# Kernel optimization log

Measured on AMD Instinct MI355X. Metric: run time of the kernel, lower is better.

Reference implementation:

```python
import jax, jax.numpy as jnp
import numpy as np

B, N, K, NB = 8, 4096, 16, 8
MAX_RADIUS = 10.0
OUT_MUL = 64  # irreps_out = '64x1o' -> output dim 64*3 = 192


def setup_inputs() -> dict:
    key = jax.random.key(0)
    k1, k2 = jax.random.split(key)
    coords = jax.random.normal(k1, (B, N, 3), dtype=jnp.float32)
    tp_weight = jax.random.normal(k2, (1, NB, OUT_MUL), dtype=jnp.float32)
    return {"coords": coords, "tp_weight": tp_weight}


def _knn_indices(coords, k):
    # coords: [B, N, 3] -> nbr idx [B, N, k] (no self loops), per-batch kNN
    n = coords.shape[1]
    d2 = jnp.sum((coords[:, :, None, :] - coords[:, None, :, :]) ** 2, axis=-1)  # [B,N,N]
    d2 = jnp.where(jnp.eye(n, dtype=bool)[None], jnp.inf, d2)
    _, idx = jax.lax.top_k(-d2, k)  # k nearest
    return idx


def reference(coords, tp_weight):
    nbr = _knn_indices(coords, K)                                # [B,N,K] int32
    nbr_coords = jax.vmap(lambda c, i: c[i])(coords, nbr)        # [B,N,K,3]
    r = nbr_coords - coords[:, :, None, :]                       # sender - receiver
    dist = jnp.linalg.norm(r, axis=-1, keepdims=True)            # [B,N,K,1]
    rhat = r / (dist + 1e-8)                                     # 1x1o input
    cutoff = jnp.clip(dist / MAX_RADIUS, 0.0, 1.0)
    # gaussian soft one-hot over [0,1] with NB centers
    centers = jnp.linspace(0.0, 1.0, NB, dtype=coords.dtype)
    sigma = 1.0 / NB
    g = jnp.exp(-((cutoff - centers) ** 2) / (2.0 * sigma * sigma))  # [B,N,K,NB]
    s = jnp.sum(g, axis=-1, keepdims=True)
    rb = g / jnp.where(s > 0, s, jnp.ones_like(s))               # 8x0e input
    # FullyConnectedTensorProduct 1x1o x NBx0e -> OUT_MULx1o (shared weights)
    # path normalization: 1/sqrt(mul_in1 * mul_in2) = 1/sqrt(NB)
    alpha = 1.0 / np.sqrt(1 * NB)
    W = tp_weight[0]                                             # [NB, OUT_MUL]
    edge_feat = alpha * jnp.einsum('vw,bnkv,bnkm->bnkwm', W, rb, rhat)  # [B,N,K,64,3]
    # exactly k incoming edges per receiver -> scatter_mean == mean over K
    agg = jnp.mean(edge_feat, axis=2).reshape(B, N, OUT_MUL * 3)  # [B,N,192]
    return agg
```

## Files before the change

### kernel.cpp

```cpp
#include <hip/hip_runtime.h>

typedef unsigned int u32;
typedef unsigned long long u64;

#define NBATCH 8
#define NPTS   4096
#define NQTOT  (NBATCH * NPTS)
#define KNN    16
#define NBASIS 8
#define OUTM   64
#define NSPLIT 8
#define SUBCH  (NPTS / NSPLIT)
#define QPB    64
#define TKNN   (QPB * NSPLIT)
#define GRP    8
#define BUFCAP 96
#define BUFSTR 97

#define SENT 0x7f800000ffffffffull

__device__ __forceinline__ void ce(u64& x, u64& y) {
  u64 a = x, b = y;
  bool sw = b < a;
  x = sw ? b : a;
  y = sw ? a : b;
}

template <int N>
__device__ __forceinline__ void oems_sort(u64* a) {
#pragma unroll
  for (int p = 1; p < N; p <<= 1) {
#pragma unroll
    for (int k = p; k >= 1; k >>= 1) {
#pragma unroll
      for (int j = k & (p - 1); j + k < N; j += 2 * k) {
#pragma unroll
        for (int i = 0; i < k; ++i) {
          int lo = i + j, hi = i + j + k;
          if (hi < N && (lo / (2 * p)) == (hi / (2 * p)))
            ce(a[lo], a[hi]);
        }
      }
    }
  }
}

__device__ __forceinline__ void merge16(u64 t[16], const u64 a[16]) {
  u64 m[16];
#pragma unroll
  for (int i = 0; i < 16; ++i) {
    u64 x = t[i], y = a[15 - i];
    m[i] = (x < y) ? x : y;
  }
#pragma unroll
  for (int k = 8; k >= 1; k >>= 1) {
#pragma unroll
    for (int i = 0; i < 16; ++i) {
      if ((i & k) == 0) ce(m[i], m[i | k]);
    }
  }
#pragma unroll
  for (int i = 0; i < 16; ++i) t[i] = m[i];
}

__global__ __launch_bounds__(TKNN, 4) void se3_kernel(
    const float* __restrict__ Xp, const float* __restrict__ Yp,
    const float* __restrict__ Zp, const float4* __restrict__ cpad,
    const float* __restrict__ Wmat, float* __restrict__ out) {
  __shared__ u64 sBuf[QPB * BUFSTR];
  __shared__ u32 sCnt[QPB];
  __shared__ float sThr[QPB];
  __shared__ float sM[QPB * 25];

  const int b = blockIdx.x;
  const int qg = blockIdx.y;
  const int tid = threadIdx.x;
  const int ql = tid & 63;
  const int sp = tid >> 6;
  const int qi = qg * QPB + ql;
  const int base = b * NPTS;

  if (tid < QPB) sCnt[tid] = 0;

  const float qx = Xp[base + qi];
  const float qy = Yp[base + qi];
  const float qz = Zp[base + qi];

  u64 t16[16];
  if (sp == 0) {
    const float4* xs4 = (const float4*)(Xp + base);
    const float4* ys4 = (const float4*)(Yp + base);
    const float4* zs4 = (const float4*)(Zp + base);
    float cx[16], cy[16], cz[16];
#pragma unroll
    for (int h = 0; h < 4; ++h) {
      float4 fx = xs4[h], fy = ys4[h], fz = zs4[h];
      cx[h * 4 + 0] = fx.x; cx[h * 4 + 1] = fx.y; cx[h * 4 + 2] = fx.z; cx[h * 4 + 3] = fx.w;
      cy[h * 4 + 0] = fy.x; cy[h * 4 + 1] = fy.y; cy[h * 4 + 2] = fy.z; cy[h * 4 + 3] = fy.w;
      cz[h * 4 + 0] = fz.x; cz[h * 4 + 1] = fz.y; cz[h * 4 + 2] = fz.z; cz[h * 4 + 3] = fz.w;
    }
#pragma unroll
    for (int i = 0; i < 16; ++i) {
      float dx = __fadd_rn(qx, -cx[i]);
      float dy = __fadd_rn(qy, -cy[i]);
      float dz = __fadd_rn(qz, -cz[i]);
      float d2 = __fadd_rn(__fadd_rn(__fmul_rn(dx, dx), __fmul_rn(dy, dy)),
                           __fmul_rn(dz, dz));
      u64 v = ((u64)__float_as_uint(d2) << 32) | (u32)i;
      t16[i] = (i == qi) ? SENT : v;
    }
    oems_sort<16>(t16);
    sThr[ql] = __uint_as_float((u32)(t16[15] >> 32));
  }
  __syncthreads();
  float thr = sThr[ql];

  const int jbase = __builtin_amdgcn_readfirstlane(sp * SUBCH);
  const float4* xs4 = (const float4*)(Xp + base + jbase);
  const float4* ys4 = (const float4*)(Yp + base + jbase);
  const float4* zs4 = (const float4*)(Zp + base + jbase);

  int done = 0;
  for (int ph = 0; ph < 7; ++ph) {
    const int until = 1 << ph;
    for (int it = done; it < until; ++it) {
      const int g = it * GRP;
      float4 fx0 = xs4[(g >> 2) + 0], fx1 = xs4[(g >> 2) + 1];
      float4 fy0 = ys4[(g >> 2) + 0], fy1 = ys4[(g >> 2) + 1];
      float4 fz0 = zs4[(g >> 2) + 0], fz1 = zs4[(g >> 2) + 1];
      float cx[GRP] = {fx0.x, fx0.y, fx0.z, fx0.w, fx1.x, fx1.y, fx1.z, fx1.w};
      float cy[GRP] = {fy0.x, fy0.y, fy0.z, fy0.w, fy1.x, fy1.y, fy1.z, fy1.w};
      float cz[GRP] = {fz0.x, fz0.y, fz0.z, fz0.w, fz1.x, fz1.y, fz1.z, fz1.w};
      float d2v[GRP];
      int want[GRP];
#pragma unroll
      for (int i = 0; i < GRP; ++i) {
        int j = jbase + g + i;
        float dx = __fadd_rn(qx, -cx[i]);
        float dy = __fadd_rn(qy, -cy[i]);
        float dz = __fadd_rn(qz, -cz[i]);
        d2v[i] = __fadd_rn(__fadd_rn(__fmul_rn(dx, dx), __fmul_rn(dy, dy)),
                           __fmul_rn(dz, dz));
        want[i] = (d2v[i] <= thr) & (j != qi) & (j >= 16);
      }
#pragma unroll
      for (int i = 0; i < GRP; ++i) {
        if (want[i]) {
          u32 slot = atomicAdd(&sCnt[ql], 1u);
          if (slot < BUFCAP)
            sBuf[ql * BUFSTR + slot] =
                ((u64)__float_as_uint(d2v[i]) << 32) | (u32)(jbase + g + i);
        }
      }
    }
    done = until;
    __syncthreads();
    if (sp == 0) {
      int n = (int)sCnt[ql];
      n = n < BUFCAP ? n : BUFCAP;
      for (int k = 0; __any(k < n); k += 16) {
        u64 a[16];
#pragma unroll
        for (int e = 0; e < 16; ++e)
          a[e] = (k + e < n) ? sBuf[ql * BUFSTR + k + e] : SENT;
        oems_sort<16>(a);
        merge16(t16, a);
      }
      sCnt[ql] = 0;
      sThr[ql] = __uint_as_float((u32)(t16[15] >> 32));
    }
    __syncthreads();
    thr = sThr[ql];
  }

  if (sp == 0) {
    float M[24];
#pragma unroll
    for (int j = 0; j < 24; ++j) M[j] = 0.f;
#pragma unroll
    for (int chk = 0; chk < 4; ++chk) {
      float4 nc[4];
      float dd[4];
#pragma unroll
      for (int e = 0; e < 4; ++e) {
        u64 v = t16[chk * 4 + e];
        nc[e] = cpad[base + (int)(u32)v];
        dd[e] = __uint_as_float((u32)(v >> 32));
      }
#pragma unroll
      for (int e = 0; e < 4; ++e) {
        float rx = nc[e].x - qx;
        float ry = nc[e].y - qy;
        float rz = nc[e].z - qz;
        float dist = sqrtf(dd[e]);
        float inv = 1.0f / (dist + 1e-8f);
        rx *= inv; ry *= inv; rz *= inv;
        float cut = fminf(dist * 0.1f, 1.0f);
        float g[NBASIS], s = 0.f;
#pragma unroll
        for (int v = 0; v < NBASIS; ++v) {
          float t = cut - (float)v * (1.0f / 7.0f);
          g[v] = __expf(-32.0f * t * t);
          s += g[v];
        }
        float rs = 1.0f / s;
#pragma unroll
        for (int v = 0; v < NBASIS; ++v) {
          float rb = g[v] * rs;
          M[v * 3 + 0] = fmaf(rb, rx, M[v * 3 + 0]);
          M[v * 3 + 1] = fmaf(rb, ry, M[v * 3 + 1]);
          M[v * 3 + 2] = fmaf(rb, rz, M[v * 3 + 2]);
        }
      }
    }
#pragma unroll
    for (int j = 0; j < 24; ++j) sM[ql * 25 + j] = M[j];
  }
  __syncthreads();

  float wreg[NBASIS];
#pragma unroll
  for (int v = 0; v < NBASIS; ++v) wreg[v] = Wmat[v * OUTM + ql];
  const float scale = 0.022097086912079608f;
#pragma unroll
  for (int i = 0; i < 8; ++i) {
    int q = sp * 8 + i;
    const float* mq = sM + q * 25;
    float a0 = 0.f, a1 = 0.f, a2 = 0.f;
#pragma unroll
    for (int v = 0; v < NBASIS; ++v) {
      a0 = fmaf(wreg[v], mq[v * 3 + 0], a0);
      a1 = fmaf(wreg[v], mq[v * 3 + 1], a1);
      a2 = fmaf(wreg[v], mq[v * 3 + 2], a2);
    }
    size_t o = (size_t)(base + qg * QPB + q) * (OUTM * 3) + ql * 3;
    out[o + 0] = a0 * scale;
    out[o + 1] = a1 * scale;
    out[o + 2] = a2 * scale;
  }
}

__global__ void prep_kernel(const float* __restrict__ coords,
                            float* __restrict__ Xp, float* __restrict__ Yp,
                            float* __restrict__ Zp, float4* __restrict__ cpad) {
  int i = blockIdx.x * 256 + threadIdx.x;
  if (i < NQTOT) {
    float x = coords[3 * i + 0];
    float y = coords[3 * i + 1];
    float z = coords[3 * i + 2];
    Xp[i] = x; Yp[i] = y; Zp[i] = z;
    cpad[i] = make_float4(x, y, z, 0.f);
  }
}

extern "C" void kernel_launch(void* const* d_in, const int* in_sizes, int n_in,
                              void* d_out, int out_size, void* d_ws, size_t ws_size,
                              hipStream_t stream) {
  const float* coords = (const float*)d_in[0];
  const float* Wmat = (const float*)d_in[1];
  float* out = (float*)d_out;

  char* w = (char*)d_ws;
  float* Xp = (float*)(w);
  float* Yp = (float*)(w + 131072);
  float* Zp = (float*)(w + 262144);
  float4* cpad = (float4*)(w + 393216);

  prep_kernel<<<dim3((NQTOT + 255) / 256), dim3(256), 0, stream>>>(coords, Xp, Yp, Zp, cpad);
  se3_kernel<<<dim3(NBATCH, NPTS / QPB), dim3(TKNN), 0, stream>>>(Xp, Yp, Zp, cpad, Wmat, out);
}
```

Measured before the change: 186.1 us.

## Use per-thread top-16 lists with shared threshold and tree merge across splits

Each of the eight split threads per query now keeps its own sorted top-16 list. It seeds that list from the first 16 points of its own window and filters candidates against a shared per-query threshold that is lowered with atomicMin. Candidates go into a private 16-slot column buffer in LDS, which is flushed and merged when it is nearly full. The eight lists are then combined with a three-level tree merge through shared memory. This removes the serialized phase loop in which only split 0 sorted every buffer. It also drops the per-candidate shared atomicAdd and uses packed 2-wide float math for the distances. In exchange, all threads now do sorting work and the thresholds stay looser early on, which can admit more candidates.

Result: slower. 235.6 us (+26.6%).

```diff
diff --git a/kernel.cpp b/kernel.cpp
--- a/kernel.cpp
+++ b/kernel.cpp
@@ -2,6 +2,7 @@
 
 typedef unsigned int u32;
 typedef unsigned long long u64;
+typedef float v2f __attribute__((ext_vector_type(2)));
 
 #define NBATCH 8
 #define NPTS   4096
@@ -10,12 +11,11 @@
 #define NBASIS 8
 #define OUTM   64
 #define NSPLIT 8
-#define SUBCH  (NPTS / NSPLIT)
+#define WIN    (NPTS / NSPLIT)
 #define QPB    64
 #define TKNN   (QPB * NSPLIT)
+#define CAP    16
 #define GRP    8
-#define BUFCAP 96
-#define BUFSTR 97
 
 #define SENT 0x7f800000ffffffffull
 
@@ -63,13 +63,33 @@
   for (int i = 0; i < 16; ++i) t[i] = m[i];
 }
 
-__global__ __launch_bounds__(TKNN, 4) void se3_kernel(
+__device__ __forceinline__ v2f d2pair(v2f cx, v2f cy, v2f cz, v2f qx, v2f qy,
+                                      v2f qz) {
+#pragma clang fp contract(off)
+  v2f dx = cx - qx;
+  v2f dy = cy - qy;
+  v2f dz = cz - qz;
+  v2f d2 = (dx * dx + dy * dy) + dz * dz;
+  return d2;
+}
+
+__device__ __forceinline__ void flush_buf(u64* col, int& c, u64 t16[16],
+                                          u32* sThrU, int ql) {
+  u64 a[16];
+#pragma unroll
+  for (int e = 0; e < 16; ++e) a[e] = (e < c) ? col[(size_t)e * TKNN] : SENT;
+  oems_sort<16>(a);
+  merge16(t16, a);
+  c = 0;
+  atomicMin(&sThrU[ql], (u32)(t16[15] >> 32));
+}
+
+__global__ __launch_bounds__(TKNN) void se3_kernel(
     const float* __restrict__ Xp, const float* __restrict__ Yp,
     const float* __restrict__ Zp, const float4* __restrict__ cpad,
     const float* __restrict__ Wmat, float* __restrict__ out) {
-  __shared__ u64 sBuf[QPB * BUFSTR];
-  __shared__ u32 sCnt[QPB];
-  __shared__ float sThr[QPB];
+  __shared__ u64 sBuf[CAP * TKNN];
+  __shared__ u32 sThrU[QPB];
   __shared__ float sM[QPB * 25];
 
   const int b = blockIdx.x;
@@ -80,97 +100,89 @@
   const int qi = qg * QPB + ql;
   const int base = b * NPTS;
 
-  if (tid < QPB) sCnt[tid] = 0;
+  if (tid < QPB) sThrU[tid] = 0x7f800000u;
 
   const float qx = Xp[base + qi];
   const float qy = Yp[base + qi];
   const float qz = Zp[base + qi];
+  const v2f qxx = {qx, qx}, qyy = {qy, qy}, qzz = {qz, qz};
+
+  const int wbase = __builtin_amdgcn_readfirstlane(sp * WIN);
+  const v2f* xs2 = (const v2f*)(Xp + base + wbase);
+  const v2f* ys2 = (const v2f*)(Yp + base + wbase);
+  const v2f* zs2 = (const v2f*)(Zp + base + wbase);
+
+  __syncthreads();
 
   u64 t16[16];
-  if (sp == 0) {
-    const float4* xs4 = (const float4*)(Xp + base);
-    const float4* ys4 = (const float4*)(Yp + base);
-    const float4* zs4 = (const float4*)(Zp + base);
-    float cx[16], cy[16], cz[16];
-#pragma unroll
-    for (int h = 0; h < 4; ++h) {
-      float4 fx = xs4[h], fy = ys4[h], fz = zs4[h];
-      cx[h * 4 + 0] = fx.x; cx[h * 4 + 1] = fx.y; cx[h * 4 + 2] = fx.z; cx[h * 4 + 3] = fx.w;
-      cy[h * 4 + 0] = fy.x; cy[h * 4 + 1] = fy.y; cy[h * 4 + 2] = fy.z; cy[h * 4 + 3] = fy.w;
-      cz[h * 4 + 0] = fz.x; cz[h * 4 + 1] = fz.y; cz[h * 4 + 2] = fz.z; cz[h * 4 + 3] = fz.w;
+  {
+    float cd[16];
+#pragma unroll
+    for (int p = 0; p < 8; ++p) {
+      v2f d2 = d2pair(xs2[p], ys2[p], zs2[p], qxx, qyy, qzz);
+      cd[2 * p + 0] = d2.x;
+      cd[2 * p + 1] = d2.y;
     }
 #pragma unroll
     for (int i = 0; i < 16; ++i) {
-      float dx = __fadd_rn(qx, -cx[i]);
-      float dy = __fadd_rn(qy, -cy[i]);
-      float dz = __fadd_rn(qz, -cz[i]);
-      float d2 = __fadd_rn(__fadd_rn(__fmul_rn(dx, dx), __fmul_rn(dy, dy)),
-                           __fmul_rn(dz, dz));
-      u64 v = ((u64)__float_as_uint(d2) << 32) | (u32)i;
-      t16[i] = (i == qi) ? SENT : v;
+      u64 v = ((u64)__float_as_uint(cd[i]) << 32) | (u32)(wbase + i);
+      t16[i] = (wbase + i == qi) ? SENT : v;
     }
     oems_sort<16>(t16);
-    sThr[ql] = __uint_as_float((u32)(t16[15] >> 32));
-  }
-  __syncthreads();
-  float thr = sThr[ql];
-
-  const int jbase = __builtin_amdgcn_readfirstlane(sp * SUBCH);
-  const float4* xs4 = (const float4*)(Xp + base + jbase);
-  const float4* ys4 = (const float4*)(Yp + base + jbase);
-  const float4* zs4 = (const float4*)(Zp + base + jbase);
-
-  int done = 0;
-  for (int ph = 0; ph < 7; ++ph) {
-    const int until = 1 << ph;
-    for (int it = done; it < until; ++it) {
-      const int g = it * GRP;
-      float4 fx0 = xs4[(g >> 2) + 0], fx1 = xs4[(g >> 2) + 1];
-      float4 fy0 = ys4[(g >> 2) + 0], fy1 = ys4[(g >> 2) + 1];
-      float4 fz0 = zs4[(g >> 2) + 0], fz1 = zs4[(g >> 2) + 1];
-      float cx[GRP] = {fx0.x, fx0.y, fx0.z, fx0.w, fx1.x, fx1.y, fx1.z, fx1.w};
-      float cy[GRP] = {fy0.x, fy0.y, fy0.z, fy0.w, fy1.x, fy1.y, fy1.z, fy1.w};
-      float cz[GRP] = {fz0.x, fz0.y, fz0.z, fz0.w, fz1.x, fz1.y, fz1.z, fz1.w};
-      float d2v[GRP];
-      int want[GRP];
+    atomicMin(&sThrU[ql], (u32)(t16[15] >> 32));
+  }
+  __syncthreads();
+
+  volatile u32* vThr = sThrU;
+  int c = 0;
+  u64* col = sBuf + tid;
+
+  for (int g = 16; g < WIN; g += GRP) {
+    v2f d2p[4];
+#pragma unroll
+    for (int p = 0; p < 4; ++p)
+      d2p[p] = d2pair(xs2[(g >> 1) + p], ys2[(g >> 1) + p], zs2[(g >> 1) + p],
+                      qxx, qyy, qzz);
+    const float thr = __uint_as_float(vThr[ql]);
+    int want = 0;
+#pragma unroll
+    for (int i = 0; i < GRP; ++i)
+      want |= (d2p[i >> 1][i & 1] <= thr) ? (1 << i) : 0;
+    if (__any(want)) {
+      if (__any(c > CAP - GRP)) flush_buf(col, c, t16, sThrU, ql);
 #pragma unroll
       for (int i = 0; i < GRP; ++i) {
-        int j = jbase + g + i;
-        float dx = __fadd_rn(qx, -cx[i]);
-        float dy = __fadd_rn(qy, -cy[i]);
-        float dz = __fadd_rn(qz, -cz[i]);
-        d2v[i] = __fadd_rn(__fadd_rn(__fmul_rn(dx, dx), __fmul_rn(dy, dy)),
-                           __fmul_rn(dz, dz));
-        want[i] = (d2v[i] <= thr) & (j != qi) & (j >= 16);
-      }
-#pragma unroll
-      for (int i = 0; i < GRP; ++i) {
-        if (want[i]) {
-          u32 slot = atomicAdd(&sCnt[ql], 1u);
-          if (slot < BUFCAP)
-            sBuf[ql * BUFSTR + slot] =
-                ((u64)__float_as_uint(d2v[i]) << 32) | (u32)(jbase + g + i);
-        }
-      }
-    }
-    done = until;
+        if (want & (1 << i)) {
+          int j = wbase + g + i;
+          if (j != qi) {
+            col[(size_t)c * TKNN] =
+                ((u64)__float_as_uint(d2p[i >> 1][i & 1]) << 32) | (u32)j;
+            c++;
+          }
+        }
+      }
+    }
+  }
+  flush_buf(col, c, t16, sThrU, ql);
+
+  __syncthreads();
+  u64* stage = sBuf;
+#pragma unroll
+  for (int h = 4; h >= 1; h >>= 1) {
+    if (sp >= h && sp < 2 * h) {
+#pragma unroll
+      for (int e = 0; e < 16; ++e)
+        stage[(size_t)((sp - h) * QPB + ql) * 17 + e] = t16[e];
+    }
     __syncthreads();
-    if (sp == 0) {
-      int n = (int)sCnt[ql];
-      n = n < BUFCAP ? n : BUFCAP;
-      for (int k = 0; __any(k < n); k += 16) {
-        u64 a[16];
-#pragma unroll
-        for (int e = 0; e < 16; ++e)
-          a[e] = (k + e < n) ? sBuf[ql * BUFSTR + k + e] : SENT;
-        oems_sort<16>(a);
-        merge16(t16, a);
-      }
-      sCnt[ql] = 0;
-      sThr[ql] = __uint_as_float((u32)(t16[15] >> 32));
+    if (sp < h) {
+      u64 a[16];
+#pragma unroll
+      for (int e = 0; e < 16; ++e)
+        a[e] = stage[(size_t)(sp * QPB + ql) * 17 + e];
+      merge16(t16, a);
     }
     __syncthreads();
-    thr = sThr[ql];
   }
 
   if (sp == 0) {
```
